# Performance work log

Measured on AMD Instinct MI355X. Metric: run time of the kernel, lower is better.

## Reference

```python
import jax, jax.numpy as jnp
import numpy as np


def setup_inputs() -> dict:
    key = jax.random.key(0)
    ks = jax.random.split(key, 8)
    B, I, H, O, K = 4096, 512, 512, 512, 16
    s = 0.02
    return {
        "sample": jax.random.normal(ks[0], (B, I), jnp.float32),
        "hiddens": jax.random.normal(ks[1], (K, B, H), jnp.float32),
        "mem_para": jax.random.uniform(ks[2], (B, H), jnp.float32),
        "Wu": jax.random.normal(ks[3], (I + H, H), jnp.float32) * s,
        "bu": jnp.zeros((H,), jnp.float32),
        "Wr": jax.random.normal(ks[4], (I + H, H), jnp.float32) * s,
        "br": jnp.zeros((H,), jnp.float32),
        "Wm": jax.random.normal(ks[5], (I + 2 * H, H), jnp.float32) * s,
        "bm": jnp.zeros((H,), jnp.float32),
        "Wh": jax.random.normal(ks[6], (I + H, H), jnp.float32) * s,
        "bh": jnp.zeros((H,), jnp.float32),
        "Wo": jax.random.normal(ks[7], (H, O), jnp.float32) * s,
        "bo": jnp.zeros((O,), jnp.float32),
    }


def _mem_filter(hiddens, mem_para):
    # hiddens: [k, B, H]; mem_para (memory gate output, 'd'): [B, H]
    # Original per-scalar recurrence: w[k]=1; w[k-1-i] = w[k-i]*(i-d)/(i+1)
    # => w[k-1-i] = cumprod_{m=0..i} (m-d)/(m+1), i.e. signed fractional binomials.
    k = hiddens.shape[0]
    i = jnp.arange(k, dtype=hiddens.dtype)[:, None, None]          # [k,1,1]
    factors = (i - mem_para[None]) / (i + 1.0)                      # [k,B,H]
    weights = jnp.flip(jnp.cumprod(factors, axis=0), axis=0)        # [k,B,H]
    return jnp.sum(hiddens * weights, axis=0)                       # [B,H]


def reference(sample, hiddens, mem_para, Wu, bu, Wr, br, Wm, bm, Wh, bh, Wo, bo):
    hidden = hiddens[-1]                                            # [B,H]
    xh = jnp.concatenate([sample, hidden], axis=1)                  # [B,I+H]
    xhd = jnp.concatenate([xh, mem_para], axis=1)                   # [B,I+2H]
    update_gate = jax.nn.sigmoid(xh @ Wu + bu)
    reset_gate = jax.nn.sigmoid(xh @ Wr + br)
    memory_gate = 0.5 * jax.nn.sigmoid(xhd @ Wm + bm)
    xrh = jnp.concatenate([sample, reset_gate * hidden], axis=1)
    h_tilde = jnp.tanh(xrh @ Wh + bh)
    hiddens_filtered = -_mem_filter(hiddens, memory_gate)
    hidden_now = hiddens_filtered + update_gate * h_tilde           # [B,H]
    updated_hiddens = jnp.concatenate([hiddens[1:], hidden_now[None]], axis=0)
    output = hidden_now @ Wo + bo                                   # [B,O]
    return (output, updated_hiddens, memory_gate)
```

## Files before the change

kernel.cpp:

```cpp
#include <hip/hip_runtime.h>
#include <math.h>

typedef __bf16 bf16;
typedef __bf16 bf16x8 __attribute__((ext_vector_type(8)));
typedef __bf16 bf16x4 __attribute__((ext_vector_type(4)));
typedef float  f32x4  __attribute__((ext_vector_type(4)));

constexpr int BATCH = 4096;
constexpr int HID   = 512;
constexpr int NSTEP = 16;
constexpr int SLICE = BATCH * HID;

__device__ __forceinline__ float sigmoidf_(float x) {
    return 1.0f / (1.0f + __expf(-x));
}
__device__ __forceinline__ float tanh_fast(float x) {
    x = fminf(fmaxf(x, -15.0f), 15.0f);
    float e = __expf(2.0f * x);
    return (e - 1.0f) / (e + 1.0f);
}

__device__ __forceinline__ void gload_lds16(const void* g, void* l) {
    __builtin_amdgcn_global_load_lds((const __attribute__((address_space(1))) void*)g,
                                     (__attribute__((address_space(3))) void*)l,
                                     16, 0, 0);
}

__global__ __launch_bounds__(256)
void prep_all(const float* __restrict__ sample,
              const float* __restrict__ hidden,
              const float* __restrict__ mem_para,
              const float* __restrict__ Wu, const float* __restrict__ Wr,
              const float* __restrict__ Wm, const float* __restrict__ Wh,
              const float* __restrict__ Wo,
              bf16* __restrict__ Sb, bf16* __restrict__ Hb, bf16* __restrict__ Mb,
              bf16* __restrict__ Wall_t, bf16* __restrict__ Wh_t,
              bf16* __restrict__ Wo_t) {
    __shared__ float tile[32][33];
    const int bid = blockIdx.x;
    if (bid < 6144) {
        const int seg = bid >> 11;
        const int i = (bid & 2047) * 256 + threadIdx.x;
        const float* in = (seg == 0) ? sample : (seg == 1) ? hidden : mem_para;
        bf16* out = (seg == 0) ? Sb : (seg == 1) ? Hb : Mb;
        float4 v = ((const float4*)in)[i];
        bf16x4 o = {(bf16)v.x, (bf16)v.y, (bf16)v.z, (bf16)v.w};
        ((bf16x4*)out)[i] = o;
        return;
    }
    const int t = bid - 6144;
    const float* in; bf16* out; int stride, row_off, t2;
    if (t < 512)        { in = Wu; out = Wall_t; stride = 1536; row_off = 0;    t2 = t; }
    else if (t < 1024)  { in = Wr; out = Wall_t; stride = 1536; row_off = 512;  t2 = t - 512; }
    else if (t < 1792)  { in = Wm; out = Wall_t; stride = 1536; row_off = 1024; t2 = t - 1024; }
    else if (t < 2304)  { in = Wh; out = Wh_t;   stride = 1024; row_off = 0;    t2 = t - 1792; }
    else                { in = Wo; out = Wo_t;   stride = 512;  row_off = 0;    t2 = t - 2304; }
    const int r0 = (t2 >> 4) * 32, c0 = (t2 & 15) * 32;
    const int tr = threadIdx.x >> 5;
    const int tc = threadIdx.x & 31;
#pragma unroll
    for (int i = 0; i < 4; ++i)
        tile[tr + i * 8][tc] = in[(size_t)(r0 + tr + i * 8) * 512 + c0 + tc];
    __syncthreads();
#pragma unroll
    for (int i = 0; i < 4; ++i) {
        const int c = tr + i * 8;
        out[(size_t)(row_off + c0 + c) * stride + r0 + tc] = (bf16)tile[tc][c];
    }
}

__global__ __launch_bounds__(256)
void gemm_urm(const bf16* __restrict__ Sb,
              const bf16* __restrict__ Hb,
              const bf16* __restrict__ Mb,
              const bf16* __restrict__ Wall_t,
              const float* __restrict__ bu,
              const float* __restrict__ br,
              const float* __restrict__ bm,
              bf16* __restrict__ UGb,
              bf16* __restrict__ RHb,
              float* __restrict__ out_mg) {
    __shared__ bf16 As[128 * 64];
    __shared__ bf16 Bs[64 * 64];

    const int tid  = threadIdx.x;
    const int wid  = tid >> 6;
    const int lane = tid & 63;
    const int wr = wid >> 1, wc = wid & 1;
    const int brow = blockIdx.x * 128;
    const int bcol = blockIdx.y * 64;

    const bf16* segs[3] = {Sb, Hb, Mb};
    const int nkt = (bcol >= 1024) ? 24 : 16;

    const int s_row  = tid >> 3;
    const int s_chnk = tid & 7;

    f32x4 acc[4][2] = {};

    for (int t = 0; t < nkt; ++t) {
        const int k0 = t * 64;
        const bf16* Aseg = segs[k0 >> 9];
        const int kloc = k0 & 511;

#pragma unroll
        for (int c = 0; c < 4; ++c) {
            const int row = c * 32 + s_row;
            const int sc  = s_chnk ^ (row & 7);
            gload_lds16(Aseg + (size_t)(brow + row) * 512 + kloc + sc * 8,
                        As + (size_t)(c * 256 + (wid << 6)) * 8);
        }
#pragma unroll
        for (int c = 0; c < 2; ++c) {
            const int row = c * 32 + s_row;
            const int sc  = s_chnk ^ (row & 7);
            gload_lds16(Wall_t + (size_t)(bcol + row) * 1536 + k0 + sc * 8,
                        Bs + (size_t)(c * 256 + (wid << 6)) * 8);
        }
        __syncthreads();

#pragma unroll
        for (int ks = 0; ks < 2; ++ks) {
            const int kb = ks * 64 + ((lane >> 4) << 4);
            bf16x8 bfrag[2];
#pragma unroll
            for (int ni = 0; ni < 2; ++ni) {
                const int n = wc * 32 + ni * 16 + (lane & 15);
                bfrag[ni] = *(const bf16x8*)((const char*)Bs +
                                             n * 128 + (kb ^ ((n & 7) << 4)));
            }
#pragma unroll
            for (int mi = 0; mi < 4; ++mi) {
                const int m = wr * 64 + mi * 16 + (lane & 15);
                const bf16x8 afrag = *(const bf16x8*)((const char*)As +
                                                      m * 128 + (kb ^ ((m & 7) << 4)));
#pragma unroll
                for (int ni = 0; ni < 2; ++ni)
                    acc[mi][ni] = __builtin_amdgcn_mfma_f32_16x16x32_bf16(
                        afrag, bfrag[ni], acc[mi][ni], 0, 0, 0);
            }
        }
        __syncthreads();
    }

    const int lr4 = (lane >> 4) * 4;
    const int lc  = lane & 15;
#pragma unroll
    for (int mi = 0; mi < 4; ++mi) {
#pragma unroll
        for (int ni = 0; ni < 2; ++ni) {
            const int col = bcol + wc * 32 + ni * 16 + lc;
            const f32x4 a = acc[mi][ni];
#pragma unroll
            for (int r = 0; r < 4; ++r) {
                const int row = brow + wr * 64 + mi * 16 + lr4 + r;
                const float x = a[r];
                if (col < 512) {
                    UGb[(size_t)row * 512 + col] = (bf16)sigmoidf_(x + bu[col]);
                } else if (col < 1024) {
                    const int c2 = col - 512;
                    const float v = sigmoidf_(x + br[c2]) *
                                    (float)Hb[(size_t)row * 512 + c2];
                    RHb[(size_t)row * 512 + c2] = (bf16)v;
                } else {
                    const int c3 = col - 1024;
                    out_mg[(size_t)row * 512 + c3] = 0.5f * sigmoidf_(x + bm[c3]);
                }
            }
        }
    }
}

template <int ACT, int KTILES>
__global__ __launch_bounds__(256)
void gemm_mfma(const bf16* __restrict__ segA0,
               const bf16* __restrict__ segA1,
               const bf16* __restrict__ Wt, int ldK,
               const float* __restrict__ b0,
               void* __restrict__ outA) {
    __shared__ bf16 As[128 * 64];
    __shared__ bf16 Bs[64 * 64];

    const int tid  = threadIdx.x;
    const int wid  = tid >> 6;
    const int lane = tid & 63;
    const int wr = wid >> 1, wc = wid & 1;
    const int brow = blockIdx.x * 128;
    const int bcol = blockIdx.y * 64;

    const bf16* segs[2] = {segA0, segA1};

    const int s_row  = tid >> 3;
    const int s_chnk = tid & 7;

    f32x4 acc[4][2] = {};

    for (int t = 0; t < KTILES; ++t) {
        const int k0 = t * 64;
        const bf16* Aseg = segs[k0 >> 9];
        const int kloc = k0 & 511;

#pragma unroll
        for (int c = 0; c < 4; ++c) {
            const int row = c * 32 + s_row;
            const int sc  = s_chnk ^ (row & 7);
            gload_lds16(Aseg + (size_t)(brow + row) * 512 + kloc + sc * 8,
                        As + (size_t)(c * 256 + (wid << 6)) * 8);
        }
#pragma unroll
        for (int c = 0; c < 2; ++c) {
            const int row = c * 32 + s_row;
            const int sc  = s_chnk ^ (row & 7);
            gload_lds16(Wt + (size_t)(bcol + row) * ldK + k0 + sc * 8,
                        Bs + (size_t)(c * 256 + (wid << 6)) * 8);
        }
        __syncthreads();

#pragma unroll
        for (int ks = 0; ks < 2; ++ks) {
            const int kb = ks * 64 + ((lane >> 4) << 4);
            bf16x8 bfrag[2];
#pragma unroll
            for (int ni = 0; ni < 2; ++ni) {
                const int n = wc * 32 + ni * 16 + (lane & 15);
                bfrag[ni] = *(const bf16x8*)((const char*)Bs +
                                             n * 128 + (kb ^ ((n & 7) << 4)));
            }
#pragma unroll
            for (int mi = 0; mi < 4; ++mi) {
                const int m = wr * 64 + mi * 16 + (lane & 15);
                const bf16x8 afrag = *(const bf16x8*)((const char*)As +
                                                      m * 128 + (kb ^ ((m & 7) << 4)));
#pragma unroll
                for (int ni = 0; ni < 2; ++ni)
                    acc[mi][ni] = __builtin_amdgcn_mfma_f32_16x16x32_bf16(
                        afrag, bfrag[ni], acc[mi][ni], 0, 0, 0);
            }
        }
        __syncthreads();
    }

    const int lr4 = (lane >> 4) * 4;
    const int lc  = lane & 15;
#pragma unroll
    for (int mi = 0; mi < 4; ++mi) {
#pragma unroll
        for (int ni = 0; ni < 2; ++ni) {
            const int col = bcol + wc * 32 + ni * 16 + lc;
            const f32x4 a = acc[mi][ni];
#pragma unroll
            for (int r = 0; r < 4; ++r) {
                const int row = brow + wr * 64 + mi * 16 + lr4 + r;
                const float x = a[r];
                if constexpr (ACT == 2) {
                    ((bf16*)outA)[(size_t)row * 512 + col] = (bf16)tanh_fast(x + b0[col]);
                } else {
                    ((float*)outA)[(size_t)row * 512 + col] = x + b0[col];
                }
            }
        }
    }
}

__global__ __launch_bounds__(256)
void filter_combine(const float* __restrict__ hiddens,
                    const bf16* __restrict__ ugb,
                    const bf16* __restrict__ htb,
                    const float* __restrict__ mg,
                    float* __restrict__ out_upd,
                    bf16* __restrict__ hnb) {
    const int idx = blockIdx.x * blockDim.x + threadIdx.x;
    const int S4 = SLICE / 4;
    const float4* h4 = (const float4*)hiddens;
    float4* o4 = (float4*)out_upd;

    const float4 d = ((const float4*)mg)[idx];
    float cx = 1.f, cy = 1.f, cz = 1.f, cw = 1.f;
    float ax = 0.f, ay = 0.f, az = 0.f, aw = 0.f;

#pragma unroll
    for (int i = 0; i < NSTEP; ++i) {
        const int j = NSTEP - 1 - i;
        const float4 v = h4[j * S4 + idx];
        const float fi = (float)i;
        const float inv = 1.0f / (float)(i + 1);
        cx *= (fi - d.x) * inv;
        cy *= (fi - d.y) * inv;
        cz *= (fi - d.z) * inv;
        cw *= (fi - d.w) * inv;
        ax = fmaf(v.x, cx, ax);
        ay = fmaf(v.y, cy, ay);
        az = fmaf(v.z, cz, az);
        aw = fmaf(v.w, cw, aw);
        if (j >= 1) o4[(j - 1) * S4 + idx] = v;
    }

    const bf16x4 u4 = ((const bf16x4*)ugb)[idx];
    const bf16x4 t4 = ((const bf16x4*)htb)[idx];
    float4 hn;
    hn.x = fmaf((float)u4[0], (float)t4[0], -ax);
    hn.y = fmaf((float)u4[1], (float)t4[1], -ay);
    hn.z = fmaf((float)u4[2], (float)t4[2], -az);
    hn.w = fmaf((float)u4[3], (float)t4[3], -aw);
    o4[(NSTEP - 1) * S4 + idx] = hn;
    bf16x4 hb = {(bf16)hn.x, (bf16)hn.y, (bf16)hn.z, (bf16)hn.w};
    ((bf16x4*)hnb)[idx] = hb;
}

extern "C" void kernel_launch(void* const* d_in, const int* in_sizes, int n_in,
                              void* d_out, int out_size, void* d_ws, size_t ws_size,
                              hipStream_t stream) {
    const float* sample   = (const float*)d_in[0];
    const float* hiddens  = (const float*)d_in[1];
    const float* mem_para = (const float*)d_in[2];
    const float* Wu = (const float*)d_in[3];
    const float* bu = (const float*)d_in[4];
    const float* Wr = (const float*)d_in[5];
    const float* br = (const float*)d_in[6];
    const float* Wm = (const float*)d_in[7];
    const float* bm = (const float*)d_in[8];
    const float* Wh = (const float*)d_in[9];
    const float* bh = (const float*)d_in[10];
    const float* Wo = (const float*)d_in[11];
    const float* bo = (const float*)d_in[12];

    float* out        = (float*)d_out;
    float* out_output = out;
    float* out_upd    = out + SLICE;
    float* out_mg     = out + SLICE + (size_t)NSTEP * SLICE;

    const float* hidden = hiddens + (size_t)(NSTEP - 1) * SLICE;

    char* ws = (char*)d_ws;
    bf16* Sb    = (bf16*)(ws);
    bf16* Hb    = (bf16*)(ws + (((size_t) 4) << 20));
    bf16* Mb    = (bf16*)(ws + (((size_t) 8) << 20));
    bf16* RHb   = (bf16*)(ws + (((size_t)12) << 20));
    bf16* HNb   = (bf16*)(ws + (((size_t)16) << 20));
    bf16* UGb   = (bf16*)(ws + (((size_t)20) << 20));
    bf16* HTb   = (bf16*)(ws + (((size_t)24) << 20));
    bf16* Wall_t = (bf16*)(ws + (((size_t)28) << 20));
    bf16* Wh_t  = (bf16*)(ws + (((size_t)33) << 20));
    bf16* Wo_t  = (bf16*)(ws + (((size_t)35) << 20));

    dim3 blk(256);
    const int n4 = SLICE / 4;

    prep_all<<<8704, blk, 0, stream>>>(sample, hidden, mem_para,
                                       Wu, Wr, Wm, Wh, Wo,
                                       Sb, Hb, Mb, Wall_t, Wh_t, Wo_t);
    gemm_urm<<<dim3(32, 24), blk, 0, stream>>>(
        Sb, Hb, Mb, Wall_t, bu, br, bm, UGb, RHb, out_mg);
    gemm_mfma<2, 16><<<dim3(32, 8), blk, 0, stream>>>(
        Sb, RHb, Wh_t, 1024, bh, HTb);
    filter_combine<<<n4 / 256, blk, 0, stream>>>(hiddens, UGb, HTb, out_mg, out_upd, HNb);
    gemm_mfma<3, 8><<<dim3(32, 8), blk, 0, stream>>>(
        HNb, nullptr, Wo_t, 512, bo, out_output);
}
```

Baseline: 130.3 us.

## Overlap memory-bound hiddens copy and filter sum with GEMM kernels

Moves the 15-slice hiddens shift-copy into extra blocks of the update/reset/memory gate GEMM launch, and the fractional-binomial filter sum into extra blocks of the Wh GEMM launch. The bandwidth-bound streaming work then runs concurrently with compute-bound MFMA tiles instead of in a separate elementwise pass after them. A small combine kernel finishes h_now using a new fp32 filt buffer in workspace. This adds an extra 8MB write and read of the filter result, and the GEMM blocks now share the device with heavy streaming traffic.

After: 130.5 us. No clear change (+0.1%).

```diff
diff --git a/kernel.cpp b/kernel.cpp
--- a/kernel.cpp
+++ b/kernel.cpp
@@ -10,6 +10,7 @@
 constexpr int HID   = 512;
 constexpr int NSTEP = 16;
 constexpr int SLICE = BATCH * HID;
+constexpr int S4    = SLICE / 4;
 
 __device__ __forceinline__ float sigmoidf_(float x) {
     return 1.0f / (1.0f + __expf(-x));
@@ -70,25 +71,42 @@
 }
 
 __global__ __launch_bounds__(256)
-void gemm_urm(const bf16* __restrict__ Sb,
-              const bf16* __restrict__ Hb,
-              const bf16* __restrict__ Mb,
-              const bf16* __restrict__ Wall_t,
-              const float* __restrict__ bu,
-              const float* __restrict__ br,
-              const float* __restrict__ bm,
-              bf16* __restrict__ UGb,
-              bf16* __restrict__ RHb,
-              float* __restrict__ out_mg) {
+void gemm_urm_copy(const bf16* __restrict__ Sb,
+                   const bf16* __restrict__ Hb,
+                   const bf16* __restrict__ Mb,
+                   const bf16* __restrict__ Wall_t,
+                   const float* __restrict__ bu,
+                   const float* __restrict__ br,
+                   const float* __restrict__ bm,
+                   bf16* __restrict__ UGb,
+                   bf16* __restrict__ RHb,
+                   float* __restrict__ out_mg,
+                   const float* __restrict__ hiddens,
+                   float* __restrict__ out_upd) {
     __shared__ bf16 As[128 * 64];
     __shared__ bf16 Bs[64 * 64];
 
-    const int tid  = threadIdx.x;
+    const int bid = blockIdx.x;
+    const int tid = threadIdx.x;
+
+    if (bid >= 768) {
+        const int base = (bid - 768) * 4096 + tid;
+        const f32x4* src = ((const f32x4*)hiddens) + S4;
+        f32x4* dst = (f32x4*)out_upd;
+#pragma unroll
+        for (int u = 0; u < 16; ++u) {
+            const int f = base + u * 256;
+            f32x4 v = __builtin_nontemporal_load(src + f);
+            __builtin_nontemporal_store(v, dst + f);
+        }
+        return;
+    }
+
     const int wid  = tid >> 6;
     const int lane = tid & 63;
     const int wr = wid >> 1, wc = wid & 1;
-    const int brow = blockIdx.x * 128;
-    const int bcol = blockIdx.y * 64;
+    const int brow = (bid & 31) * 128;
+    const int bcol = (bid >> 5) * 64;
 
     const bf16* segs[3] = {Sb, Hb, Mb};
     const int nkt = (bcol >= 1024) ? 24 : 16;
@@ -171,13 +189,139 @@
     }
 }
 
-template <int ACT, int KTILES>
 __global__ __launch_bounds__(256)
-void gemm_mfma(const bf16* __restrict__ segA0,
-               const bf16* __restrict__ segA1,
-               const bf16* __restrict__ Wt, int ldK,
-               const float* __restrict__ b0,
-               void* __restrict__ outA) {
+void gemm_wh_sum(const bf16* __restrict__ Sb,
+                 const bf16* __restrict__ RHb,
+                 const bf16* __restrict__ Wh_t,
+                 const float* __restrict__ bh,
+                 bf16* __restrict__ HTb,
+                 const float* __restrict__ hiddens,
+                 const float* __restrict__ mg,
+                 float* __restrict__ filt) {
+    __shared__ bf16 As[128 * 64];
+    __shared__ bf16 Bs[64 * 64];
+
+    const int bid = blockIdx.x;
+    const int tid = threadIdx.x;
+
+    if (bid >= 256) {
+        const int idx = (bid - 256) * 256 + tid;
+        const f32x4 d = ((const f32x4*)mg)[idx];
+        f32x4 c = {1.f, 1.f, 1.f, 1.f};
+        f32x4 a = {0.f, 0.f, 0.f, 0.f};
+#pragma unroll
+        for (int i = 0; i < NSTEP; ++i) {
+            const int j = NSTEP - 1 - i;
+            const f32x4 v = __builtin_nontemporal_load(
+                ((const f32x4*)hiddens) + (size_t)j * S4 + idx);
+            const float fi = (float)i;
+            const float inv = 1.0f / (float)(i + 1);
+            c *= (fi - d) * inv;
+            a += v * c;
+        }
+        __builtin_nontemporal_store(a, ((f32x4*)filt) + idx);
+        return;
+    }
+
+    const int wid  = tid >> 6;
+    const int lane = tid & 63;
+    const int wr = wid >> 1, wc = wid & 1;
+    const int brow = (bid & 31) * 128;
+    const int bcol = (bid >> 5) * 64;
+
+    const bf16* segs[2] = {Sb, RHb};
+
+    const int s_row  = tid >> 3;
+    const int s_chnk = tid & 7;
+
+    f32x4 acc[4][2] = {};
+
+    for (int t = 0; t < 16; ++t) {
+        const int k0 = t * 64;
+        const bf16* Aseg = segs[k0 >> 9];
+        const int kloc = k0 & 511;
+
+#pragma unroll
+        for (int c = 0; c < 4; ++c) {
+            const int row = c * 32 + s_row;
+            const int sc  = s_chnk ^ (row & 7);
+            gload_lds16(Aseg + (size_t)(brow + row) * 512 + kloc + sc * 8,
+                        As + (size_t)(c * 256 + (wid << 6)) * 8);
+        }
+#pragma unroll
+        for (int c = 0; c < 2; ++c) {
+            const int row = c * 32 + s_row;
+            const int sc  = s_chnk ^ (row & 7);
+            gload_lds16(Wh_t + (size_t)(bcol + row) * 1024 + k0 + sc * 8,
+                        Bs + (size_t)(c * 256 + (wid << 6)) * 8);
+        }
+        __syncthreads();
+
+#pragma unroll
+        for (int ks = 0; ks < 2; ++ks) {
+            const int kb = ks * 64 + ((lane >> 4) << 4);
+            bf16x8 bfrag[2];
+#pragma unroll
+            for (int ni = 0; ni < 2; ++ni) {
+                const int n = wc * 32 + ni * 16 + (lane & 15);
+                bfrag[ni] = *(const bf16x8*)((const char*)Bs +
+                                             n * 128 + (kb ^ ((n & 7) << 4)));
+            }
+#pragma unroll
+            for (int mi = 0; mi < 4; ++mi) {
+                const int m = wr * 64 + mi * 16 + (lane & 15);
+                const bf16x8 afrag = *(const bf16x8*)((const char*)As +
+                                                      m * 128 + (kb ^ ((m & 7) << 4)));
+#pragma unroll
+                for (int ni = 0; ni < 2; ++ni)
+                    acc[mi][ni] = __builtin_amdgcn_mfma_f32_16x16x32_bf16(
+                        afrag, bfrag[ni], acc[mi][ni], 0, 0, 0);
+            }
+        }
+        __syncthreads();
+    }
+
+    const int lr4 = (lane >> 4) * 4;
+    const int lc  = lane & 15;
+#pragma unroll
+    for (int mi = 0; mi < 4; ++mi) {
+#pragma unroll
+        for (int ni = 0; ni < 2; ++ni) {
+            const int col = bcol + wc * 32 + ni * 16 + lc;
+            const f32x4 a = acc[mi][ni];
+#pragma unroll
+            for (int r = 0; r < 4; ++r) {
+                const int row = brow + wr * 64 + mi * 16 + lr4 + r;
+                HTb[(size_t)row * 512 + col] = (bf16)tanh_fast(a[r] + bh[col]);
+            }
+        }
+    }
+}
+
+__global__ __launch_bounds__(256)
+void combine(const float* __restrict__ filt,
+             const bf16* __restrict__ ugb,
+             const bf16* __restrict__ htb,
+             float* __restrict__ out_upd,
+             bf16* __restrict__ hnb) {
+    const int idx = blockIdx.x * 256 + threadIdx.x;
+    const f32x4 a = ((const f32x4*)filt)[idx];
+    const bf16x4 u = ((const bf16x4*)ugb)[idx];
+    const bf16x4 t = ((const bf16x4*)htb)[idx];
+    f32x4 hn;
+#pragma unroll
+    for (int e = 0; e < 4; ++e)
+        hn[e] = fmaf((float)u[e], (float)t[e], -a[e]);
+    ((f32x4*)out_upd)[(size_t)(NSTEP - 1) * S4 + idx] = hn;
+    bf16x4 hb = {(bf16)hn[0], (bf16)hn[1], (bf16)hn[2], (bf16)hn[3]};
+    ((bf16x4*)hnb)[idx] = hb;
+}
+
+__global__ __launch_bounds__(256)
+void gemm_out(const bf16* __restrict__ HNb,
+              const bf16* __restrict__ Wo_t,
+              const float* __restrict__ bo,
+              float* __restrict__ outp) {
     __shared__ bf16 As[128 * 64];
     __shared__ bf16 Bs[64 * 64];
 
@@ -188,30 +332,26 @@
     const int brow = blockIdx.x * 128;
     const int bcol = blockIdx.y * 64;
 
-    const bf16* segs[2] = {segA0, segA1};
-
     const int s_row  = tid >> 3;
     const int s_chnk = tid & 7;
 
     f32x4 acc[4][2] = {};
 
-    for (int t = 0; t < KTILES; ++t) {
+    for (int t = 0; t < 8; ++t) {
         const int k0 = t * 64;
-        const bf16* Aseg = segs[k0 >> 9];
-        const int kloc = k0 & 511;
 
 #pragma unroll
         for (int c = 0; c < 4; ++c) {
             const int row = c * 32 + s_row;
             const int sc  = s_chnk ^ (row & 7);
-            gload_lds16(Aseg + (size_t)(brow + row) * 512 + kloc + sc * 8,
+            gload_lds16(HNb + (size_t)(brow + row) * 512 + k0 + sc * 8,
                         As + (size_t)(c * 256 + (wid << 6)) * 8);
         }
 #pragma unroll
         for (int c = 0; c < 2; ++c) {
             const int row = c * 32 + s_row;
             const int sc  = s_chnk ^ (row & 7);
-            gload_lds16(Wt + (size_t)(bcol + row) * ldK + k0 + sc * 8,
+            gload_lds16(Wo_t + (size_t)(bcol + row) * 512 + k0 + sc * 8,
                         Bs + (size_t)(c * 256 + (wid << 6)) * 8);
         }
         __syncthreads();
@@ -251,60 +391,10 @@
 #pragma unroll
             for (int r = 0; r < 4; ++r) {
                 const int row = brow + wr * 64 + mi * 16 + lr4 + r;
-                const float x = a[r];
-                if constexpr (ACT == 2) {
-                    ((bf16*)outA)[(size_t)row * 512 + col] = (bf16)tanh_fast(x + b0[col]);
-                } else {
-                    ((float*)outA)[(size_t)row * 512 + col] = x + b0[col];
-                }
-            }
-        }
-    }
-}
-
-__global__ __launch_bounds__(256)
-void filter_combine(const float* __restrict__ hiddens,
-                    const bf16* __restrict__ ugb,
-                    const bf16* __restrict__ htb,
-                    const float* __restrict__ mg,
-                    float* __restrict__ out_upd,
-                    bf16* __restrict__ hnb) {
-    const int idx = blockIdx.x * blockDim.x + threadIdx.x;
-    const int S4 = SLICE / 4;
-    const float4* h4 = (const float4*)hiddens;
-    float4* o4 = (float4*)out_upd;
-
-    const float4 d = ((const float4*)mg)[idx];
-    float cx = 1.f, cy = 1.f, cz = 1.f, cw = 1.f;
-    float ax = 0.f, ay = 0.f, az = 0.f, aw = 0.f;
-
-#pragma unroll
-    for (int i = 0; i < NSTEP; ++i) {
-        const int j = NSTEP - 1 - i;
-        const float4 v = h4[j * S4 + idx];
-        const float fi = (float)i;
-        const float inv = 1.0f / (float)(i + 1);
-        cx *= (fi - d.x) * inv;
-        cy *= (fi - d.y) * inv;
-        cz *= (fi - d.z) * inv;
-        cw *= (fi - d.w) * inv;
-        ax = fmaf(v.x, cx, ax);
-        ay = fmaf(v.y, cy, ay);
-        az = fmaf(v.z, cz, az);
-        aw = fmaf(v.w, cw, aw);
-        if (j >= 1) o4[(j - 1) * S4 + idx] = v;
-    }
-
-    const bf16x4 u4 = ((const bf16x4*)ugb)[idx];
-    const bf16x4 t4 = ((const bf16x4*)htb)[idx];
-    float4 hn;
-    hn.x = fmaf((float)u4[0], (float)t4[0], -ax);
-    hn.y = fmaf((float)u4[1], (float)t4[1], -ay);
-    hn.z = fmaf((float)u4[2], (float)t4[2], -az);
-    hn.w = fmaf((float)u4[3], (float)t4[3], -aw);
-    o4[(NSTEP - 1) * S4 + idx] = hn;
-    bf16x4 hb = {(bf16)hn.x, (bf16)hn.y, (bf16)hn.z, (bf16)hn.w};
-    ((bf16x4*)hnb)[idx] = hb;
+                outp[(size_t)row * 512 + col] = a[r] + bo[col];
+            }
+        }
+    }
 }
 
 extern "C" void kernel_launch(void* const* d_in, const int* in_sizes, int n_in,
@@ -342,18 +432,17 @@
     bf16* Wall_t = (bf16*)(ws + (((size_t)28) << 20));
     bf16* Wh_t  = (bf16*)(ws + (((size_t)33) << 20));
     bf16* Wo_t  = (bf16*)(ws + (((size_t)35) << 20));
+    float* filt = (float*)(ws + (((size_t)40) << 20));
 
     dim3 blk(256);
-    const int n4 = SLICE / 4;
 
     prep_all<<<8704, blk, 0, stream>>>(sample, hidden, mem_para,
                                        Wu, Wr, Wm, Wh, Wo,
                                        Sb, Hb, Mb, Wall_t, Wh_t, Wo_t);
-    gemm_urm<<<dim3(32, 24), blk, 0, stream>>>(
-        Sb, Hb, Mb, Wall_t, bu, br, bm, UGb, RHb, out_mg);
-    gemm_mfma<2, 16><<<dim3(32, 8), blk, 0, stream>>>(
-        Sb, RHb, Wh_t, 1024, bh, HTb);
-    filter_combine<<<n4 / 256, blk, 0, stream>>>(hiddens, UGb, HTb, out_mg, out_upd, HNb);
-    gemm_mfma<3, 8><<<dim3(32, 8), blk, 0, stream>>>(
-        HNb, nullptr, Wo_t, 512, bo, out_output);
-}
+    gemm_urm_copy<<<768 + 1920, blk, 0, stream>>>(
+        Sb, Hb, Mb, Wall_t, bu, br, bm, UGb, RHb, out_mg, hiddens, out_upd);
+    gemm_wh_sum<<<256 + 2048, blk, 0, stream>>>(
+        Sb, RHb, Wh_t, bh, HTb, hiddens, out_mg, filt);
+    combine<<<S4 / 256, blk, 0, stream>>>(filt, UGb, HTb, out_upd, HNb);
+    gemm_out<<<dim3(32, 8), blk, 0, stream>>>(HNb, Wo_t, bo, out_output);
+}
```
